# Kernel optimization log

Measured on AMD Instinct MI355X. Metric: run time of the kernel, lower is better.

Reference implementation:

```python
import jax, jax.numpy as jnp
import numpy as np

B, L, PD, D, H, NB, NC = 32, 256, 164, 240, 16, 6, 250
DK = D // H            # 15
HID = 2 * D            # FeedForward hidden = out_dim*2 = 480
SCALE = 1.0 / float(np.sqrt(DK))
MAXLEN = 256


def _pos_embed(length, d):
    half = d // 2
    position = np.arange(length)[:, None]
    dim = np.arange(half)[None, :] / half
    angle = position * (1.0 / 1000.0 ** dim)
    return np.concatenate([np.sin(angle), np.cos(angle)], axis=-1).astype(np.float32)


def _ln(x, g, b, eps=1e-5):
    m = jnp.mean(x, axis=-1, keepdims=True)
    v = jnp.mean((x - m) ** 2, axis=-1, keepdims=True)
    return (x - m) * jax.lax.rsqrt(v + eps) * g + b


def setup_inputs() -> dict:
    key = jax.random.key(0)
    ks = iter(jax.random.split(key, 16))
    p = lambda shape: (jax.random.normal(next(ks), shape) * 0.02).astype(jnp.float32)
    z = lambda shape: jnp.zeros(shape, jnp.float32)
    o = lambda shape: jnp.ones(shape, jnp.float32)
    return {
        "x": jax.random.normal(next(ks), (B, L, PD), dtype=jnp.float32),
        "pos_embed": jnp.asarray(_pos_embed(MAXLEN, D)),
        "cls_embed": z((1, D)),
        "e_W1": p((PD, 2 * D)), "e_b1": z((2 * D,)), "e_g1": o((2 * D,)), "e_bn1": z((2 * D,)),
        "e_W2": p((2 * D, D)), "e_b2": z((D,)), "e_g2": o((D,)), "e_bn2": z((D,)),
        "ln1_g": o((NB, D)), "ln1_b": z((NB, D)),
        "Wq": p((NB, D, D)), "bq": z((NB, D)),
        "Wk": p((NB, D, D)), "bk": z((NB, D)),
        "Wv": p((NB, D, D)), "bv": z((NB, D)),
        "Wo": p((NB, D, D)), "bo": z((NB, D)),
        "ln2_g": o((NB, D)), "ln2_b": z((NB, D)),
        "W1": p((NB, D, HID)), "b1": z((NB, HID)),
        "W2": p((NB, HID, D)), "b2": z((NB, D)),
        "logit_W": p((D, NC)), "logit_b": z((NC,)),
    }


def reference(x, pos_embed, cls_embed,
              e_W1, e_b1, e_g1, e_bn1, e_W2, e_b2, e_g2, e_bn2,
              ln1_g, ln1_b, Wq, bq, Wk, bk, Wv, bv, Wo, bo,
              ln2_g, ln2_b, W1, b1, W2, b2, logit_W, logit_b):
    # padding mask: True where token is padding (all-zero features -> max == 0)
    pad = jnp.max(x, axis=2) == 0                      # [B, L]
    # XEmbed
    h = jax.nn.relu(_ln(x @ e_W1 + e_b1, e_g1, e_bn1))
    h = jax.nn.relu(_ln(h @ e_W2 + e_b2, e_g2, e_bn2))  # [B, L, D]
    h = h + pos_embed[:L][None]
    h = jnp.concatenate([jnp.broadcast_to(cls_embed[None], (B, 1, D)), h], axis=1)
    mask = jnp.concatenate([jnp.zeros((B, 1), bool), pad], axis=1)  # [B, L+1]
    Lp = L + 1
    for i in range(NB):
        # pre-norm attention (residual)
        y = _ln(h, ln1_g[i], ln1_b[i])
        q = (y @ Wq[i] + bq[i]).reshape(B, Lp, H, DK)
        k = (y @ Wk[i] + bk[i]).reshape(B, Lp, H, DK)
        v = (y @ Wv[i] + bv[i]).reshape(B, Lp, H, DK)
        scores = jnp.einsum('bqhd,bkhd->bhqk', q, k) * SCALE
        scores = jnp.where(mask[:, None, None, :], -10000.0, scores)
        attn = jax.nn.softmax(scores, axis=-1)
        o = jnp.einsum('bhqk,bkhd->bqhd', attn, v).reshape(B, Lp, D)
        h = h + (o @ Wo[i] + bo[i])
        # pre-norm FFN (residual)
        z2 = _ln(h, ln2_g[i], ln2_b[i])
        h = h + (jax.nn.relu(z2 @ W1[i] + b1[i]) @ W2[i] + b2[i])
    # masked mean pool over valid tokens (CLS always valid)
    w = (~mask).astype(h.dtype)[:, :, None]
    last = (h * w).sum(axis=1) / w.sum(axis=1)
    return last @ logit_W + logit_b                    # [B, NC]
```

## Files before the change

kernel.cpp:

```cpp
#include <hip/hip_runtime.h>
#include <math.h>

#define B_  32
#define L_  256
#define PD_ 164
#define D_  240
#define H_  16
#define NB_ 6
#define NC_ 250
#define DK_ 15
#define HID_ 480
#define LP_ 257
#define KP_ 288
#define SCALE_ 0.2581988897471611f
#define LOG2E_ 1.4426950408889634f

typedef __attribute__((ext_vector_type(8))) short bf16x8;
typedef __attribute__((ext_vector_type(8))) _Float16 f16x8;
typedef __attribute__((ext_vector_type(4))) float f32x4;

static __device__ inline unsigned short f2bf(float x) {
    unsigned u = __builtin_bit_cast(unsigned, x);
    u += 0x7FFFu + ((u >> 16) & 1u);
    return (unsigned short)(u >> 16);
}
static __device__ inline unsigned short f2h(float x) {
    _Float16 h = (_Float16)x;
    return __builtin_bit_cast(unsigned short, h);
}

static __device__ inline void gl2lds16(const void* g, void* l) {
    __builtin_amdgcn_global_load_lds(
        (const __attribute__((address_space(1))) unsigned int*)g,
        (__attribute__((address_space(3))) unsigned int*)l, 16, 0, 0);
}

__global__ void prep_misc(const float* __restrict__ x, unsigned short* __restrict__ xbf,
                          const float* __restrict__ bq, const float* __restrict__ bk,
                          const float* __restrict__ bv, float* __restrict__ b720,
                          float* __restrict__ mask) {
    int u = blockIdx.x;
    if (u < 8192) {
        const float* src = x + (size_t)u * PD_;
        unsigned short* dst = xbf + (size_t)u * 192;
        for (int k = threadIdx.x; k < 192; k += 64)
            dst[k] = f2bf(k < PD_ ? src[k] : 0.f);
    } else if (u < 8192 + NB_) {
        int i = u - 8192;
        for (int n = threadIdx.x; n < 720; n += 64) {
            float v = (n < 240) ? bq[i * 240 + n]
                    : (n < 480) ? bk[i * 240 + n - 240]
                                : bv[i * 240 + n - 480];
            b720[i * 720 + n] = v;
        }
    } else {
        int idx = (u - 8192 - NB_) * 64 + threadIdx.x;
        if (idx >= B_ * LP_) return;
        int b = idx / LP_, l = idx % LP_;
        if (l == 0) { mask[idx] = 0.f; return; }
        const float4* xr = (const float4*)(x + ((size_t)b * L_ + (l - 1)) * PD_);
        float4 m4 = xr[0];
        #pragma unroll 8
        for (int j = 1; j < 41; j++) {
            float4 v = xr[j];
            m4.x = fmaxf(m4.x, v.x); m4.y = fmaxf(m4.y, v.y);
            m4.z = fmaxf(m4.z, v.z); m4.w = fmaxf(m4.w, v.w);
        }
        float mx = fmaxf(fmaxf(m4.x, m4.y), fmaxf(m4.z, m4.w));
        mask[idx] = (mx == 0.f) ? 1.f : 0.f;
    }
}

__global__ __launch_bounds__(256)
void prep_weights(const float* __restrict__ e_W1, const float* __restrict__ e_W2,
                  const float* __restrict__ Wq, const float* __restrict__ Wk,
                  const float* __restrict__ Wv, const float* __restrict__ Wo,
                  const float* __restrict__ W1, const float* __restrict__ W2,
                  unsigned short* __restrict__ We1, unsigned short* __restrict__ We2,
                  unsigned short* __restrict__ Wqkv, unsigned short* __restrict__ WoT,
                  unsigned short* __restrict__ W1T, unsigned short* __restrict__ W2T) {
    int job = blockIdx.y;
    const float* src; unsigned short* dst; int K, N, Kpad;
    if (job == 0)      { src = e_W1; dst = We1; K = PD_; N = 480; Kpad = 192; }
    else if (job == 1) { src = e_W2; dst = We2; K = 480; N = 240; Kpad = 480; }
    else {
        int i = (job - 2) % 6, w = (job - 2) / 6;
        if (w == 0)      { src = Wq + (size_t)i*240*240; dst = Wqkv + (size_t)i*768*256;           K=240; N=240; Kpad=256; }
        else if (w == 1) { src = Wk + (size_t)i*240*240; dst = Wqkv + (size_t)i*768*256 + 240*256; K=240; N=240; Kpad=256; }
        else if (w == 2) { src = Wv + (size_t)i*240*240; dst = Wqkv + (size_t)i*768*256 + 480*256; K=240; N=240; Kpad=256; }
        else if (w == 3) { src = Wo + (size_t)i*240*240; dst = WoT + (size_t)i*256*256;            K=240; N=256; Kpad=256; }
        else if (w == 4) { src = W1 + (size_t)i*240*480; dst = W1T + (size_t)i*512*256;            K=240; N=480; Kpad=256; }
        else             { src = W2 + (size_t)i*480*240; dst = W2T + (size_t)i*256*480;            K=480; N=256; Kpad=480; }
    }
    int n0 = blockIdx.x * 64;
    if (n0 >= N) return;
    int realN = (N == 256) ? 240 : N;
    __shared__ float tile[64][65];
    const int tid = threadIdx.x;
    const int lrow = tid >> 4;
    const int lcol = (tid & 15) * 4;
    const int wn   = tid >> 2;
    const int wq   = tid & 3;
    for (int k0 = 0; k0 < Kpad; k0 += 64) {
        #pragma unroll
        for (int r4 = 0; r4 < 4; r4++) {
            int row = k0 + r4 * 16 + lrow;
            float4 v = {0.f, 0.f, 0.f, 0.f};
            if (row < K && n0 + lcol < realN)
                v = *(const float4*)(src + (size_t)row * realN + n0 + lcol);
            tile[r4 * 16 + lrow][lcol]     = v.x;
            tile[r4 * 16 + lrow][lcol + 1] = v.y;
            tile[r4 * 16 + lrow][lcol + 2] = v.z;
            tile[r4 * 16 + lrow][lcol + 3] = v.w;
        }
        __syncthreads();
        int n = n0 + wn;
        int kbase = k0 + wq * 16;
        if (n < N && kbase < Kpad) {
            unsigned short tmp[16];
            #pragma unroll
            for (int kk = 0; kk < 16; kk++)
                tmp[kk] = f2bf(tile[wq * 16 + kk][wn]);
            *(uint4*)(dst + (size_t)n * Kpad + kbase)     = *(uint4*)&tmp[0];
            *(uint4*)(dst + (size_t)n * Kpad + kbase + 8) = *(uint4*)&tmp[8];
        }
        __syncthreads();
    }
}

__global__ __launch_bounds__(256)
void gemm_mfma(const unsigned short* __restrict__ A,
               const unsigned short* __restrict__ Bt,
               const float* __restrict__ bias,
               float* __restrict__ C, unsigned short* __restrict__ Cbf,
               unsigned short* __restrict__ qp, unsigned short* __restrict__ kp,
               unsigned short* __restrict__ vp,
               int M, int N, int Kpad, int Cstride, int flags)
{
    __shared__ __align__(16) unsigned short As[2][128 * 32];
    __shared__ __align__(16) unsigned short Bs[2][64 * 32];
    const int tid = threadIdx.x;
    const int gx = gridDim.x, gy = gridDim.y;
    const int flat = blockIdx.x + gx * blockIdx.y;
    const int total = gx * gy;
    const int q8 = total >> 3, r8 = total & 7;
    const int cx = flat & 7, kx = flat >> 3;
    const int w = (cx < r8) ? (cx * (q8 + 1) + kx)
                            : (r8 * (q8 + 1) + (cx - r8) * q8 + kx);
    const int bmx = w / gy;
    const int bny = w - bmx * gy;
    const int bm = bmx * 128;
    const int bn = bny * 64;
    const int zs = gridDim.z, zi = blockIdx.z;
    const int wave = tid >> 6, lane = tid & 63;
    const int wm = (wave & 1) * 64, wn = (wave >> 1) * 32;
    const int lq = lane >> 4, lr = lane & 15;

    f32x4 acc[4][2];
    #pragma unroll
    for (int i = 0; i < 4; i++)
        #pragma unroll
        for (int j = 0; j < 2; j++) acc[i][j] = (f32x4){0.f, 0.f, 0.f, 0.f};

    const int srow = lane >> 2;
    const int schk = (lane & 3) << 3;
    const int nkt = Kpad >> 5;
    const int kt0 = (nkt * zi) / zs;
    const int kt1 = (nkt * (zi + 1)) / zs;

    const unsigned short* ga0 = A + (size_t)(bm + wave * 32 + srow) * Kpad + schk + kt0 * 32;
    const unsigned short* ga1 = A + (size_t)(bm + wave * 32 + 16 + srow) * Kpad + schk + kt0 * 32;
    const unsigned short* gb  = Bt + (size_t)(bn + wave * 16 + srow) * Kpad + schk + kt0 * 32;
    char* sa = (char*)As + wave * 2048;
    char* sb = (char*)Bs + wave * 1024;

    #define STAGE_(bu)  do {                       \
        gl2lds16(ga0, sa + (bu) * 8192);           \
        gl2lds16(ga1, sa + (bu) * 8192 + 1024);    \
        gl2lds16(gb,  sb + (bu) * 4096);           \
        ga0 += 32; ga1 += 32; gb += 32;            \
    } while (0)

    STAGE_(0);
    int cur = 0;
    for (int kt = kt0; kt < kt1; kt++) {
        if (kt + 1 < kt1) {
            STAGE_(cur ^ 1);
            asm volatile("s_waitcnt vmcnt(3)" ::: "memory");
        } else {
            asm volatile("s_waitcnt vmcnt(0)" ::: "memory");
        }
        asm volatile("s_barrier" ::: "memory");
        const unsigned short* Asc = (const unsigned short*)((const char*)As + cur * 8192);
        const unsigned short* Bsc = (const unsigned short*)((const char*)Bs + cur * 4096);
        bf16x8 af[4], bfr[2];
        #pragma unroll
        for (int i = 0; i < 4; i++)
            af[i] = *(const bf16x8*)&Asc[(wm + i * 16 + lr) * 32 + lq * 8];
        #pragma unroll
        for (int j = 0; j < 2; j++)
            bfr[j] = *(const bf16x8*)&Bsc[(wn + j * 16 + lr) * 32 + lq * 8];
        #pragma unroll
        for (int i = 0; i < 4; i++)
            #pragma unroll
            for (int j = 0; j < 2; j++)
                acc[i][j] = __builtin_amdgcn_mfma_f32_16x16x32_bf16(af[i], bfr[j], acc[i][j], 0, 0, 0);
        asm volatile("s_barrier" ::: "memory");
        cur ^= 1;
    }
    #undef STAGE_

    if (flags & 4) {
        #pragma unroll
        for (int j = 0; j < 2; j++) {
            int n = bn + wn + j * 16 + lr;
            if (n >= N) continue;
            int which = n / 240;
            int rem = n - which * 240;
            int hh = rem / 15;
            int c = rem - hh * 15;
            unsigned short* dst = (which == 0) ? qp : (which == 1) ? kp : vp;
            float bias_n = bias[n];
            float mult = (which == 0) ? (SCALE_ * LOG2E_) : 1.f;
            #pragma unroll
            for (int i = 0; i < 4; i++)
                #pragma unroll
                for (int r = 0; r < 4; r++) {
                    int m = bm + wm + i * 16 + lq * 4 + r;
                    if (m >= M) continue;
                    float s = (acc[i][j][r] + bias_n) * mult;
                    int b = m / LP_, l = m - b * LP_;
                    unsigned short bits = (which == 2) ? f2h(s) : f2bf(s);
                    dst[(((size_t)b * H_ + hh) * LP_ + l) * 16 + c] = bits;
                }
        }
    } else if (flags & 8) {
        #pragma unroll
        for (int i = 0; i < 4; i++)
            #pragma unroll
            for (int j = 0; j < 2; j++) {
                int n = bn + wn + j * 16 + lr;
                if (n >= N) continue;
                float bias_n = bias ? bias[n] : 0.f;
                #pragma unroll
                for (int r = 0; r < 4; r++) {
                    int m = bm + wm + i * 16 + lq * 4 + r;
                    if (m >= M) continue;
                    float s = acc[i][j][r] + bias_n;
                    if (flags & 1) s = fmaxf(s, 0.f);
                    Cbf[(size_t)m * Cstride + n] = f2bf(s);
                }
            }
    } else {
        #pragma unroll
        for (int i = 0; i < 4; i++)
            #pragma unroll
            for (int j = 0; j < 2; j++) {
                int n = bn + wn + j * 16 + lr;
                if (n >= N) continue;
                float bias_n = (bias && zi == 0) ? bias[n] : 0.f;
                #pragma unroll
                for (int r = 0; r < 4; r++) {
                    int m = bm + wm + i * 16 + lq * 4 + r;
                    if (m >= M) continue;
                    float s = acc[i][j][r] + bias_n;
                    if (flags & 1) s = fmaxf(s, 0.f);
                    size_t off = (size_t)m * Cstride + n;
                    if (flags & 2) {
                        if (zs > 1) atomicAdd(&C[off], s);
                        else C[off] += s;
                    } else C[off] = s;
                }
            }
    }
}

__global__ __launch_bounds__(256)
void ln240(const float* __restrict__ in, unsigned short* __restrict__ out,
           const float* __restrict__ g, const float* __restrict__ bb) {
    const int row = blockIdx.x * 4 + (threadIdx.x >> 6);
    const int lane = threadIdx.x & 63;
    const float* x = in + (size_t)row * 240;
    float4 v = {0.f, 0.f, 0.f, 0.f};
    if (lane < 60) v = *(const float4*)(x + lane * 4);
    float s = (v.x + v.y) + (v.z + v.w);
    #pragma unroll
    for (int off = 32; off; off >>= 1) s += __shfl_xor(s, off);
    const float mean = s * (1.f / 240.f);
    float4 d;
    d.x = v.x - mean; d.y = v.y - mean; d.z = v.z - mean; d.w = v.w - mean;
    float vs = (lane < 60) ? (d.x * d.x + d.y * d.y) + (d.z * d.z + d.w * d.w) : 0.f;
    #pragma unroll
    for (int off = 32; off; off >>= 1) vs += __shfl_xor(vs, off);
    const float rs = rsqrtf(vs * (1.f / 240.f) + 1e-5f);
    ushort4 o4 = {0, 0, 0, 0};
    if (lane < 60) {
        float4 g4 = *(const float4*)(g + lane * 4);
        float4 b4 = *(const float4*)(bb + lane * 4);
        o4.x = f2bf(d.x * rs * g4.x + b4.x);
        o4.y = f2bf(d.y * rs * g4.y + b4.y);
        o4.z = f2bf(d.z * rs * g4.z + b4.z);
        o4.w = f2bf(d.w * rs * g4.w + b4.w);
    }
    *(ushort4*)(out + (size_t)row * 256 + lane * 4) = o4;
}

__global__ __launch_bounds__(256)
void ln480(const float* __restrict__ in, unsigned short* __restrict__ out,
           const float* __restrict__ g, const float* __restrict__ bb) {
    const int row = blockIdx.x * 4 + (threadIdx.x >> 6);
    const int lane = threadIdx.x & 63;
    const float* x = in + (size_t)row * 480;
    float4 va = {0.f,0.f,0.f,0.f}, vb = {0.f,0.f,0.f,0.f};
    if (lane < 60) {
        va = *(const float4*)(x + lane * 8);
        vb = *(const float4*)(x + lane * 8 + 4);
    }
    float s = ((va.x + va.y) + (va.z + va.w)) + ((vb.x + vb.y) + (vb.z + vb.w));
    #pragma unroll
    for (int off = 32; off; off >>= 1) s += __shfl_xor(s, off);
    const float mean = s * (1.f / 480.f);
    float4 da, db;
    da.x = va.x - mean; da.y = va.y - mean; da.z = va.z - mean; da.w = va.w - mean;
    db.x = vb.x - mean; db.y = vb.y - mean; db.z = vb.z - mean; db.w = vb.w - mean;
    float vs = (lane < 60) ? ((da.x*da.x + da.y*da.y) + (da.z*da.z + da.w*da.w)) +
                             ((db.x*db.x + db.y*db.y) + (db.z*db.z + db.w*db.w)) : 0.f;
    #pragma unroll
    for (int off = 32; off; off >>= 1) vs += __shfl_xor(vs, off);
    const float rs = rsqrtf(vs * (1.f / 480.f) + 1e-5f);
    if (lane < 60) {
        float4 ga = *(const float4*)(g + lane * 8);
        float4 gb = *(const float4*)(g + lane * 8 + 4);
        float4 ba = *(const float4*)(bb + lane * 8);
        float4 b2 = *(const float4*)(bb + lane * 8 + 4);
        ushort4 oa, ob;
        oa.x = f2bf(fmaxf(da.x * rs * ga.x + ba.x, 0.f));
        oa.y = f2bf(fmaxf(da.y * rs * ga.y + ba.y, 0.f));
        oa.z = f2bf(fmaxf(da.z * rs * ga.z + ba.z, 0.f));
        oa.w = f2bf(fmaxf(da.w * rs * ga.w + ba.w, 0.f));
        ob.x = f2bf(fmaxf(db.x * rs * gb.x + b2.x, 0.f));
        ob.y = f2bf(fmaxf(db.y * rs * gb.y + b2.y, 0.f));
        ob.z = f2bf(fmaxf(db.z * rs * gb.z + b2.z, 0.f));
        ob.w = f2bf(fmaxf(db.w * rs * gb.w + b2.w, 0.f));
        *(ushort4*)(out + (size_t)row * 480 + lane * 8) = oa;
        *(ushort4*)(out + (size_t)row * 480 + lane * 8 + 4) = ob;
    }
}

__global__ __launch_bounds__(256)
void embed_finish(const float* __restrict__ tmp, const float* __restrict__ mask,
                  const float* __restrict__ g, const float* __restrict__ bb,
                  const float* __restrict__ pos, const float* __restrict__ cls,
                  const float* __restrict__ l1g, const float* __restrict__ l1b,
                  float* __restrict__ h, unsigned short* __restrict__ ybf,
                  unsigned short* __restrict__ qp, unsigned short* __restrict__ kp,
                  unsigned short* __restrict__ vp) {
    const int row = blockIdx.x * 4 + (threadIdx.x >> 6);
    const int lane = threadIdx.x & 63;
    const int b = row / LP_, l = row - b * LP_;
    float* outr = h + (size_t)row * 240;

    if (lane >= 60 && lane <= 62) {
        unsigned short bits;
        unsigned short* dst;
        if (lane == 60) { bits = f2bf(LOG2E_); dst = qp; }
        else if (lane == 61) { bits = (mask[row] != 0.f) ? f2bf(-10000.f) : 0; dst = kp; }
        else { bits = f2h(1.f); dst = vp; }
        #pragma unroll
        for (int hh = 0; hh < H_; hh++)
            dst[(((size_t)b * H_ + hh) * LP_ + l) * 16 + 15] = bits;
    }

    float4 o = {0.f, 0.f, 0.f, 0.f};
    if (l == 0) {
        if (lane < 60) o = *(const float4*)(cls + lane * 4);
    } else {
        const float* x = tmp + ((size_t)b * L_ + (l - 1)) * 240;
        float4 v = {0.f, 0.f, 0.f, 0.f};
        if (lane < 60) v = *(const float4*)(x + lane * 4);
        float s = (v.x + v.y) + (v.z + v.w);
        #pragma unroll
        for (int off = 32; off; off >>= 1) s += __shfl_xor(s, off);
        const float mean = s * (1.f / 240.f);
        float4 d;
        d.x = v.x - mean; d.y = v.y - mean; d.z = v.z - mean; d.w = v.w - mean;
        float vs = (lane < 60) ? (d.x * d.x + d.y * d.y) + (d.z * d.z + d.w * d.w) : 0.f;
        #pragma unroll
        for (int off = 32; off; off >>= 1) vs += __shfl_xor(vs, off);
        const float rs = rsqrtf(vs * (1.f / 240.f) + 1e-5f);
        if (lane < 60) {
            float4 g4 = *(const float4*)(g + lane * 4);
            float4 b4 = *(const float4*)(bb + lane * 4);
            float4 p4 = *(const float4*)(pos + (size_t)(l - 1) * 240 + lane * 4);
            o.x = fmaxf(d.x * rs * g4.x + b4.x, 0.f) + p4.x;
            o.y = fmaxf(d.y * rs * g4.y + b4.y, 0.f) + p4.y;
            o.z = fmaxf(d.z * rs * g4.z + b4.z, 0.f) + p4.z;
            o.w = fmaxf(d.w * rs * g4.w + b4.w, 0.f) + p4.w;
        }
    }
    if (lane < 60) *(float4*)(outr + lane * 4) = o;

    float s1 = (o.x + o.y) + (o.z + o.w);
    #pragma unroll
    for (int off = 32; off; off >>= 1) s1 += __shfl_xor(s1, off);
    const float mean1 = s1 * (1.f / 240.f);
    float4 d1;
    d1.x = o.x - mean1; d1.y = o.y - mean1; d1.z = o.z - mean1; d1.w = o.w - mean1;
    float vs1 = (lane < 60) ? (d1.x * d1.x + d1.y * d1.y) + (d1.z * d1.z + d1.w * d1.w) : 0.f;
    #pragma unroll
    for (int off = 32; off; off >>= 1) vs1 += __shfl_xor(vs1, off);
    const float rs1 = rsqrtf(vs1 * (1.f / 240.f) + 1e-5f);
    ushort4 o4 = {0, 0, 0, 0};
    if (lane < 60) {
        float4 g4 = *(const float4*)(l1g + lane * 4);
        float4 b4 = *(const float4*)(l1b + lane * 4);
        o4.x = f2bf(d1.x * rs1 * g4.x + b4.x);
        o4.y = f2bf(d1.y * rs1 * g4.y + b4.y);
        o4.z = f2bf(d1.z * rs1 * g4.z + b4.z);
        o4.w = f2bf(d1.w * rs1 * g4.w + b4.w);
    }
    *(ushort4*)(ybf + (size_t)row * 256 + lane * 4) = o4;
}

__global__ __launch_bounds__(256)
void attn_mfma(const unsigned short* __restrict__ qp, const unsigned short* __restrict__ kp,
               const unsigned short* __restrict__ vp, unsigned short* __restrict__ obf)
{
    __shared__ __align__(16) unsigned short Kl[KP_ * 24];
    __shared__ __align__(16) unsigned short Vt[16 * 296];
    __shared__ __align__(16) unsigned short Pl[4][16 * 296];
    const int hh = blockIdx.x, b = blockIdx.y;
    const int tid = threadIdx.x;
    const int wave = tid >> 6, lane = tid & 63;
    const int lq = lane >> 4, lr = lane & 15;
    const size_t base = ((size_t)b * H_ + hh) * LP_ * 16;

    for (int key = tid; key < KP_; key += 256) {
        uint4 z = {0u, 0u, 0u, 0u};
        uint4 k0 = z, k1 = z, v0 = z, v1 = z;
        if (key < LP_) {
            k0 = *(const uint4*)(kp + base + (size_t)key * 16);
            k1 = *(const uint4*)(kp + base + (size_t)key * 16 + 8);
            v0 = *(const uint4*)(vp + base + (size_t)key * 16);
            v1 = *(const uint4*)(vp + base + (size_t)key * 16 + 8);
        } else {
            k1.w = 0xC61C0000u;
        }
        *(uint4*)&Kl[key * 24] = k0;
        *(uint4*)&Kl[key * 24 + 8] = k1;
        unsigned short vs[8];
        *(uint4*)vs = v0;
        #pragma unroll
        for (int d = 0; d < 8; d++) Vt[d * 296 + key] = vs[d];
        *(uint4*)vs = v1;
        #pragma unroll
        for (int d = 0; d < 8; d++) Vt[(d + 8) * 296 + key] = vs[d];
    }
    __syncthreads();

    unsigned short* Pw = &Pl[wave][0];
    {
        int r = lane >> 2, c0 = 272 + (lane & 3) * 4;
        ushort4 z4 = {0, 0, 0, 0};
        *(ushort4*)&Pw[r * 296 + c0] = z4;
    }
    for (int qt = wave; qt < 17; qt += 4) {
        const int qrow = qt * 16 + lr;
        bf16x8 aq = {0, 0, 0, 0, 0, 0, 0, 0};
        if (lq < 2)
            aq = *(const bf16x8*)(qp + base + (size_t)qrow * 16 + lq * 8);
        for (int kt = 0; kt < 17; kt++) {
            bf16x8 bk = {0, 0, 0, 0, 0, 0, 0, 0};
            if (lq < 2)
                bk = *(const bf16x8*)&Kl[(kt * 16 + lr) * 24 + lq * 8];
            f32x4 sacc = {0.f, 0.f, 0.f, 0.f};
            sacc = __builtin_amdgcn_mfma_f32_16x16x32_bf16(aq, bk, sacc, 0, 0, 0);
            #pragma unroll
            for (int r = 0; r < 4; r++)
                Pw[(lq * 4 + r) * 296 + kt * 16 + lr] = f2h(exp2f(sacc[r]));
        }
        asm volatile("s_waitcnt lgkmcnt(0)" ::: "memory");
        f32x4 o = {0.f, 0.f, 0.f, 0.f};
        __builtin_amdgcn_s_setprio(1);
        #pragma unroll
        for (int ks = 0; ks < 9; ks++) {
            f16x8 ap = *(const f16x8*)&Pw[lr * 296 + ks * 32 + lq * 8];
            f16x8 bv = *(const f16x8*)&Vt[lr * 296 + ks * 32 + lq * 8];
            o = __builtin_amdgcn_mfma_f32_16x16x32_f16(ap, bv, o, 0, 0, 0);
        }
        __builtin_amdgcn_s_setprio(0);
        asm volatile("s_waitcnt lgkmcnt(0)" ::: "memory");
        #pragma unroll
        for (int r = 0; r < 4; r++) {
            float denom = __shfl(o[r], lane | 15);
            int q = qt * 16 + lq * 4 + r;
            if (q < LP_ && lr < 15)
                obf[((size_t)b * LP_ + q) * 256 + hh * DK_ + lr] = f2bf(o[r] / denom);
        }
    }
    if (hh == 0) {
        for (int q = tid; q < LP_; q += 256) {
            uint4 z = {0u, 0u, 0u, 0u};
            *(uint4*)(obf + ((size_t)b * LP_ + q) * 256 + 240) = z;
            *(uint4*)(obf + ((size_t)b * LP_ + q) * 256 + 248) = z;
        }
    }
}

__global__ void pool_partial(const float* __restrict__ h, const float* __restrict__ mask,
                             float* __restrict__ partial) {
    int b = blockIdx.x, slice = blockIdx.y;
    int d = threadIdx.x;
    if (d >= D_) return;
    float s = 0.f;
    int l0 = slice * 29;
    for (int i = 0; i < 29; i++) {
        int l = l0 + i;
        if (l < LP_ && mask[b * LP_ + l] == 0.f)
            s += h[((size_t)b * LP_ + l) * D_ + d];
    }
    partial[((size_t)b * 9 + slice) * D_ + d] = s;
}

__global__ __launch_bounds__(256)
void pool_logits(const float* __restrict__ partial, const float* __restrict__ mask,
                 const float* __restrict__ W, const float* __restrict__ bias,
                 float* __restrict__ out) {
    int b = blockIdx.x;
    int t = threadIdx.x;
    __shared__ float red[256];
    __shared__ float pool[240];
    float c = 0.f;
    for (int l = t; l < LP_; l += 256) c += (mask[b * LP_ + l] == 0.f) ? 1.f : 0.f;
    red[t] = c;
    __syncthreads();
    for (int off = 128; off > 0; off >>= 1) {
        if (t < off) red[t] += red[t + off];
        __syncthreads();
    }
    float inv = 1.f / red[0];
    if (t < D_) {
        float s = 0.f;
        #pragma unroll
        for (int sl = 0; sl < 9; sl++) s += partial[((size_t)b * 9 + sl) * D_ + t];
        pool[t] = s * inv;
    }
    __syncthreads();
    if (t < NC_) {
        float s = bias[t];
        for (int kk = 0; kk < D_; kk++) s += pool[kk] * W[(size_t)kk * NC_ + t];
        out[b * NC_ + t] = s;
    }
}

extern "C" void kernel_launch(void* const* d_in, const int* in_sizes, int n_in,
                              void* d_out, int out_size, void* d_ws, size_t ws_size,
                              hipStream_t stream) {
    const float* x        = (const float*)d_in[0];
    const float* pos      = (const float*)d_in[1];
    const float* cls      = (const float*)d_in[2];
    const float* e_W1     = (const float*)d_in[3];
    const float* e_b1     = (const float*)d_in[4];
    const float* e_g1     = (const float*)d_in[5];
    const float* e_bn1    = (const float*)d_in[6];
    const float* e_W2     = (const float*)d_in[7];
    const float* e_b2     = (const float*)d_in[8];
    const float* e_g2     = (const float*)d_in[9];
    const float* e_bn2    = (const float*)d_in[10];
    const float* ln1_g    = (const float*)d_in[11];
    const float* ln1_b    = (const float*)d_in[12];
    const float* Wq       = (const float*)d_in[13];
    const float* bq       = (const float*)d_in[14];
    const float* Wk       = (const float*)d_in[15];
    const float* bk       = (const float*)d_in[16];
    const float* Wv       = (const float*)d_in[17];
    const float* bv       = (const float*)d_in[18];
    const float* Wo       = (const float*)d_in[19];
    const float* bo       = (const float*)d_in[20];
    const float* ln2_g    = (const float*)d_in[21];
    const float* ln2_b    = (const float*)d_in[22];
    const float* W1       = (const float*)d_in[23];
    const float* b1       = (const float*)d_in[24];
    const float* W2       = (const float*)d_in[25];
    const float* b2       = (const float*)d_in[26];
    const float* logit_W  = (const float*)d_in[27];
    const float* logit_b  = (const float*)d_in[28];
    float* out = (float*)d_out;

    const size_t TOK  = (size_t)B_ * LP_;
    const size_t TOKP = 8320;
    const size_t HN   = TOK * D_;
    const size_t QN   = (size_t)B_ * H_ * LP_ * 16;

    char* wsb = (char*)d_ws;
    size_t cur = 0;
    auto take = [&](size_t bytes) { void* p = wsb + cur; cur += (bytes + 15) & ~15ULL; return p; };
    float* mask = (float*)take(8224 * 4);
    float* h    = (float*)take(HN * 4);
    float* b720 = (float*)take(NB_ * 720 * 4);
    float* part = (float*)take((size_t)B_ * 9 * D_ * 4);
    void* regionA = take((size_t)8192 * 480 * 4);
    float* tmp1 = (float*)regionA;
    unsigned short* tbf = (unsigned short*)regionA;
    void* regionB = take(TOKP * 256 * 2 * 2);
    float* y32 = (float*)regionB;
    unsigned short* ybf = (unsigned short*)regionB;
    unsigned short* obf = ybf + TOKP * 256;
    unsigned short* xbf  = (unsigned short*)take((size_t)8192 * 192 * 2);
    unsigned short* We1  = (unsigned short*)take((size_t)512 * 192 * 2);
    unsigned short* We2  = (unsigned short*)take((size_t)256 * 480 * 2);
    unsigned short* Wqkv = (unsigned short*)take((size_t)NB_ * 768 * 256 * 2);
    unsigned short* WoT  = (unsigned short*)take((size_t)NB_ * 256 * 256 * 2);
    unsigned short* W1T  = (unsigned short*)take((size_t)NB_ * 512 * 256 * 2);
    unsigned short* W2T  = (unsigned short*)take((size_t)NB_ * 256 * 480 * 2);
    unsigned short* qp = (unsigned short*)take(QN * 3 * 2 + 16 * 16 * 2);
    unsigned short* kp = qp + QN;
    unsigned short* vp = kp + QN;
    unsigned short* t480bf = qp;

    const int BS = 256;

    prep_misc<<<8192 + NB_ + 129, 64, 0, stream>>>(x, xbf, bq, bk, bv, b720, mask);
    prep_weights<<<dim3(8, 38), BS, 0, stream>>>(e_W1, e_W2, Wq, Wk, Wv, Wo, W1, W2,
                                                 We1, We2, Wqkv, WoT, W1T, W2T);

    gemm_mfma<<<dim3(64, 8), BS, 0, stream>>>(xbf, We1, e_b1, tmp1, nullptr,
                                              nullptr, nullptr, nullptr,
                                              8192, 480, 192, 480, 0);
    ln480<<<2048, BS, 0, stream>>>(tmp1, t480bf, e_g1, e_bn1);
    gemm_mfma<<<dim3(64, 4), BS, 0, stream>>>(t480bf, We2, e_b2, y32, nullptr,
                                              nullptr, nullptr, nullptr,
                                              8192, 240, 480, 240, 0);
    embed_finish<<<(int)(TOK / 4), BS, 0, stream>>>(y32, mask, e_g2, e_bn2, pos, cls,
                                                    ln1_g, ln1_b, h, ybf, qp, kp, vp);

    for (int i = 0; i < NB_; i++) {
        gemm_mfma<<<dim3(65, 12), BS, 0, stream>>>(ybf, Wqkv + (size_t)i * 768 * 256,
                                                   b720 + i * 720, nullptr, nullptr,
                                                   qp, kp, vp,
                                                   (int)TOK, 720, 256, 0, 4);
        attn_mfma<<<dim3(H_, B_), BS, 0, stream>>>(qp, kp, vp, obf);
        gemm_mfma<<<dim3(65, 4, 2), BS, 0, stream>>>(obf, WoT + (size_t)i * 256 * 256,
                                                     bo + i * D_, h, nullptr,
                                                     nullptr, nullptr, nullptr,
                                                     (int)TOK, 240, 256, 240, 2);
        ln240<<<(int)(TOK / 4), BS, 0, stream>>>(h, ybf, ln2_g + i * D_, ln2_b + i * D_);
        gemm_mfma<<<dim3(65, 8), BS, 0, stream>>>(ybf, W1T + (size_t)i * 512 * 256,
                                                  b1 + i * HID_, nullptr, tbf,
                                                  nullptr, nullptr, nullptr,
                                                  (int)TOK, 480, 256, 480, 1 | 8);
        gemm_mfma<<<dim3(65, 4, 2), BS, 0, stream>>>(tbf, W2T + (size_t)i * 256 * 480,
                                                     b2 + i * D_, h, nullptr,
                                                     nullptr, nullptr, nullptr,
                                                     (int)TOK, 240, 480, 240, 2);
        if (i < NB_ - 1)
            ln240<<<(int)(TOK / 4), BS, 0, stream>>>(h, ybf,
                                                     ln1_g + (i + 1) * D_,
                                                     ln1_b + (i + 1) * D_);
    }

    pool_partial<<<dim3(B_, 9), BS, 0, stream>>>(h, mask, part);
    pool_logits<<<B_, BS, 0, stream>>>(part, mask, logit_W, logit_b, out);
}
```

Baseline: 801.4 us.

## Fuse residual-add output GEMMs with following LayerNorm via full-row tiles

Replaces the Wo and W2 projection GEMMs plus the separate ln240 launches with a single kernel that computes full 240-wide output rows per 128-row block. It adds bias and residual, writes h, and computes the LayerNorm into the bf16 buffer in the epilogue. This removes two kernel launches per block and the extra read of h, and drops the split-K atomics. The cost is a grid of only 65 blocks, down from 520, and a large per-thread accumulator array, which lowers parallelism and may raise register pressure.

```diff
diff --git a/kernel.cpp b/kernel.cpp
--- a/kernel.cpp
+++ b/kernel.cpp
@@ -276,33 +276,112 @@
 }
 
 __global__ __launch_bounds__(256)
-void ln240(const float* __restrict__ in, unsigned short* __restrict__ out,
-           const float* __restrict__ g, const float* __restrict__ bb) {
-    const int row = blockIdx.x * 4 + (threadIdx.x >> 6);
-    const int lane = threadIdx.x & 63;
-    const float* x = in + (size_t)row * 240;
-    float4 v = {0.f, 0.f, 0.f, 0.f};
-    if (lane < 60) v = *(const float4*)(x + lane * 4);
-    float s = (v.x + v.y) + (v.z + v.w);
+void gemm_row_ln(const unsigned short* __restrict__ A,
+                 const unsigned short* __restrict__ Bt,
+                 const float* __restrict__ bias,
+                 float* __restrict__ h, unsigned short* __restrict__ ybf,
+                 const float* __restrict__ lng, const float* __restrict__ lnb,
+                 int M, int Kpad, int flags)
+{
+    __shared__ __align__(16) unsigned short As[2][128 * 32];
+    __shared__ __align__(16) unsigned short Bs[2][256 * 32];
+    const int tid = threadIdx.x;
+    const int bm = blockIdx.x * 128;
+    const int wave = tid >> 6, lane = tid & 63;
+    const int wm = wave * 32;
+    const int lq = lane >> 4, lr = lane & 15;
+    const int srow = lane >> 2, schk = (lane & 3) << 3;
+    const int nkt = Kpad >> 5;
+
+    f32x4 acc[2][16];
     #pragma unroll
-    for (int off = 32; off; off >>= 1) s += __shfl_xor(s, off);
-    const float mean = s * (1.f / 240.f);
-    float4 d;
-    d.x = v.x - mean; d.y = v.y - mean; d.z = v.z - mean; d.w = v.w - mean;
-    float vs = (lane < 60) ? (d.x * d.x + d.y * d.y) + (d.z * d.z + d.w * d.w) : 0.f;
+    for (int i = 0; i < 2; i++)
+        #pragma unroll
+        for (int j = 0; j < 16; j++) acc[i][j] = (f32x4){0.f, 0.f, 0.f, 0.f};
+
+    const unsigned short* ga0 = A + (size_t)(bm + wm + srow) * Kpad + schk;
+    const unsigned short* ga1 = A + (size_t)(bm + wm + 16 + srow) * Kpad + schk;
+    const unsigned short* gb0 = Bt + (size_t)(wave * 64 + srow) * Kpad + schk;
+    char* sa = (char*)As + wave * 2048;
+    char* sb = (char*)Bs + wave * 4096;
+
+    #define STAGE_(bu)  do {                                      \
+        gl2lds16(ga0, sa + (bu) * 8192);                          \
+        gl2lds16(ga1, sa + (bu) * 8192 + 1024);                   \
+        gl2lds16(gb0,                   sb + (bu) * 16384);       \
+        gl2lds16(gb0 + (size_t)16*Kpad, sb + (bu) * 16384 + 1024);\
+        gl2lds16(gb0 + (size_t)32*Kpad, sb + (bu) * 16384 + 2048);\
+        gl2lds16(gb0 + (size_t)48*Kpad, sb + (bu) * 16384 + 3072);\
+        ga0 += 32; ga1 += 32; gb0 += 32;                          \
+    } while (0)
+
+    STAGE_(0);
+    int cur = 0;
+    for (int kt = 0; kt < nkt; kt++) {
+        if (kt + 1 < nkt) {
+            STAGE_(cur ^ 1);
+            asm volatile("s_waitcnt vmcnt(6)" ::: "memory");
+        } else {
+            asm volatile("s_waitcnt vmcnt(0)" ::: "memory");
+        }
+        asm volatile("s_barrier" ::: "memory");
+        const unsigned short* Asc = (const unsigned short*)((const char*)As + cur * 8192);
+        const unsigned short* Bsc = (const unsigned short*)((const char*)Bs + cur * 16384);
+        bf16x8 af[2];
+        #pragma unroll
+        for (int i = 0; i < 2; i++)
+            af[i] = *(const bf16x8*)&Asc[(wm + i * 16 + lr) * 32 + lq * 8];
+        #pragma unroll
+        for (int j = 0; j < 16; j++) {
+            bf16x8 bf = *(const bf16x8*)&Bsc[(j * 16 + lr) * 32 + lq * 8];
+            acc[0][j] = __builtin_amdgcn_mfma_f32_16x16x32_bf16(af[0], bf, acc[0][j], 0, 0, 0);
+            acc[1][j] = __builtin_amdgcn_mfma_f32_16x16x32_bf16(af[1], bf, acc[1][j], 0, 0, 0);
+        }
+        asm volatile("s_barrier" ::: "memory");
+        cur ^= 1;
+    }
+    #undef STAGE_
+
+    float biasj[15], gj[15], bj[15];
     #pragma unroll
-    for (int off = 32; off; off >>= 1) vs += __shfl_xor(vs, off);
-    const float rs = rsqrtf(vs * (1.f / 240.f) + 1e-5f);
-    ushort4 o4 = {0, 0, 0, 0};
-    if (lane < 60) {
-        float4 g4 = *(const float4*)(g + lane * 4);
-        float4 b4 = *(const float4*)(bb + lane * 4);
-        o4.x = f2bf(d.x * rs * g4.x + b4.x);
-        o4.y = f2bf(d.y * rs * g4.y + b4.y);
-        o4.z = f2bf(d.z * rs * g4.z + b4.z);
-        o4.w = f2bf(d.w * rs * g4.w + b4.w);
-    }
-    *(ushort4*)(out + (size_t)row * 256 + lane * 4) = o4;
+    for (int j = 0; j < 15; j++) {
+        int n = j * 16 + lr;
+        biasj[j] = bias[n];
+        if (flags & 1) { gj[j] = lng[n]; bj[j] = lnb[n]; }
+    }
+    #pragma unroll
+    for (int i = 0; i < 2; i++)
+        #pragma unroll
+        for (int r = 0; r < 4; r++) {
+            const int row = bm + wm + i * 16 + lq * 4 + r;
+            if (row >= M) continue;
+            float v[15];
+            float s = 0.f;
+            #pragma unroll
+            for (int j = 0; j < 15; j++) {
+                v[j] = acc[i][j][r] + biasj[j] + h[(size_t)row * 240 + j * 16 + lr];
+                s += v[j];
+            }
+            s += __shfl_xor(s, 1); s += __shfl_xor(s, 2);
+            s += __shfl_xor(s, 4); s += __shfl_xor(s, 8);
+            #pragma unroll
+            for (int j = 0; j < 15; j++)
+                h[(size_t)row * 240 + j * 16 + lr] = v[j];
+            if (flags & 1) {
+                const float mean = s * (1.f / 240.f);
+                float q = 0.f;
+                #pragma unroll
+                for (int j = 0; j < 15; j++) { float d = v[j] - mean; q += d * d; }
+                q += __shfl_xor(q, 1); q += __shfl_xor(q, 2);
+                q += __shfl_xor(q, 4); q += __shfl_xor(q, 8);
+                const float rs = rsqrtf(q * (1.f / 240.f) + 1e-5f);
+                #pragma unroll
+                for (int j = 0; j < 15; j++)
+                    ybf[(size_t)row * 256 + j * 16 + lr] =
+                        f2bf((v[j] - mean) * rs * gj[j] + bj[j]);
+                ybf[(size_t)row * 256 + 240 + lr] = 0;
+            }
+        }
 }
 
 __global__ __launch_bounds__(256)
@@ -640,23 +719,19 @@
                                                    qp, kp, vp,
                                                    (int)TOK, 720, 256, 0, 4);
         attn_mfma<<<dim3(H_, B_), BS, 0, stream>>>(qp, kp, vp, obf);
-        gemm_mfma<<<dim3(65, 4, 2), BS, 0, stream>>>(obf, WoT + (size_t)i * 256 * 256,
-                                                     bo + i * D_, h, nullptr,
-                                                     nullptr, nullptr, nullptr,
-                                                     (int)TOK, 240, 256, 240, 2);
-        ln240<<<(int)(TOK / 4), BS, 0, stream>>>(h, ybf, ln2_g + i * D_, ln2_b + i * D_);
+        gemm_row_ln<<<65, BS, 0, stream>>>(obf, WoT + (size_t)i * 256 * 256,
+                                           bo + i * D_, h, ybf,
+                                           ln2_g + i * D_, ln2_b + i * D_,
+                                           (int)TOK, 256, 1);
         gemm_mfma<<<dim3(65, 8), BS, 0, stream>>>(ybf, W1T + (size_t)i * 512 * 256,
                                                   b1 + i * HID_, nullptr, tbf,
                                                   nullptr, nullptr, nullptr,
                                                   (int)TOK, 480, 256, 480, 1 | 8);
-        gemm_mfma<<<dim3(65, 4, 2), BS, 0, stream>>>(tbf, W2T + (size_t)i * 256 * 480,
-                                                     b2 + i * D_, h, nullptr,
-                                                     nullptr, nullptr, nullptr,
-                                                     (int)TOK, 240, 480, 240, 2);
-        if (i < NB_ - 1)
-            ln240<<<(int)(TOK / 4), BS, 0, stream>>>(h, ybf,
-                                                     ln1_g + (i + 1) * D_,
-                                                     ln1_b + (i + 1) * D_);
+        gemm_row_ln<<<65, BS, 0, stream>>>(tbf, W2T + (size_t)i * 256 * 480,
+                                           b2 + i * D_, h, ybf,
+                                           ln1_g + ((i + 1) % NB_) * D_,
+                                           ln1_b + ((i + 1) % NB_) * D_,
+                                           (int)TOK, 480, (i < NB_ - 1) ? 1 : 0);
     }
 
     pool_partial<<<dim3(B_, 9), BS, 0, stream>>>(h, mask, part);
```

Result: faster. 781.2 us (-2.5%).
